# Optimization experiments

Hardware: AMD Instinct MI355X
Metric: run time of the kernel (lower is better)

The kernel has to match this reference:

```python
import jax, jax.numpy as jnp
import numpy as np

NUM_ITERATIONS = 3


def squash(s):
    # s: [..., out_channels]; norm over last axis (matches torch squash on squeezed tensor)
    norm = jnp.linalg.norm(s, axis=-1, keepdims=True)
    return (norm ** 2 / (1.0 + norm ** 2)) * (s / norm)


def setup_inputs() -> dict:
    key = jax.random.key(0)
    k1, k2 = jax.random.split(key)
    B, R, C, O, I = 256, 192, 96, 16, 20
    x = jax.random.normal(k1, (B, R, I), dtype=jnp.float32)
    W = jax.random.normal(k2, (R, C, O, I), dtype=jnp.float32)
    return {"x": x, "W": W}


def reference(x, W):
    # u_hat[b,r,c,o] = W[r,c,o,i] @ x[b,r,i]  (torch: matmul(W, x[i]) per batch element)
    u_hat = jnp.einsum('rcoi,bri->brco', W, x)  # [B,R,C,O]
    R, C = W.shape[0], W.shape[1]
    b_ij = jnp.zeros((R, C), dtype=x.dtype)  # shared across batch (torch b_ij is [1,R,C,1])
    v_j = None
    for it in range(NUM_ITERATIONS):
        c_ij = jax.nn.softmax(b_ij, axis=0)                 # softmax over routes (dim=1 in torch)
        s_j = jnp.einsum('rc,brco->bco', c_ij, u_hat)        # weighted sum over routes
        v_j = squash(s_j)                                    # [B,C,O]
        if it < NUM_ITERATIONS - 1:
            # agreement: <u_hat, v_j> averaged over batch (torch mean(dim=0))
            a_ij = jnp.einsum('brco,bco->rc', u_hat, v_j) / x.shape[0]
            b_ij = b_ij + a_ij
    return v_j  # [B, num_capsules, out_channels] (torch returns trailing singleton [B,C,O,1])
```

## Files before the change

### kernel.cpp

```cpp
#include <hip/hip_runtime.h>


#define R_ 192
#define C_ 96
#define O_ 16
#define I_ 20
#define B_ 256
#define K1 3840
#define N_ 1536
#define ZSPLIT 15
#define KCH 256
#define STILE 393216

typedef unsigned short u16;
typedef __attribute__((ext_vector_type(8))) short short8;
typedef __attribute__((ext_vector_type(4))) float floatx4;

__device__ inline float bf2f(u16 h) {
  union { unsigned int u; float f; } x; x.u = ((unsigned int)h) << 16; return x.f;
}
__device__ inline u16 f2bf(float f) {
  union { float f; unsigned int u; } x; x.f = f;
  unsigned int r = x.u + 0x7FFFu + ((x.u >> 16) & 1u);
  return (u16)(r >> 16);
}
__device__ inline unsigned int pack2(float a, float b) {
  return (unsigned int)f2bf(a) | ((unsigned int)f2bf(b) << 16);
}
__device__ inline void async16(const u16* g, u16* l) {
  __builtin_amdgcn_global_load_lds(
      (__attribute__((address_space(1))) void*)(unsigned long long)g,
      (__attribute__((address_space(3))) void*)(unsigned int)(unsigned long long)l,
      16, 0, 0);
}

__global__ void k_prep(const float* __restrict__ W, const float* __restrict__ X,
                       u16* __restrict__ WtT, u16* __restrict__ Xk,
                       u16* __restrict__ xT, float* __restrict__ bij) {
  int bid = blockIdx.x;
  if (bid < 5760) {
    int t = (bid * 256 + threadIdx.x) << 2;
    int n = t / K1, k = t - n * K1;
    int c = n >> 4, o = n & 15;
    const float* Wn = W + (size_t)(c * O_ + o) * I_;
    u16 h[4];
    #pragma unroll
    for (int e = 0; e < 4; ++e) {
      int ke = k + e, r = ke / I_, i = ke - r * I_;
      h[e] = f2bf(Wn[(size_t)r * (C_ * O_ * I_) + i]);
    }
    ushort4 o4; o4.x = h[0]; o4.y = h[1]; o4.z = h[2]; o4.w = h[3];
    *(ushort4*)&WtT[t] = o4;
  } else if (bid < 6000) {
    __shared__ u16 tile[64][72];
    int idx = bid - 5760;
    int kb = (idx % 60) << 6, bb = (idx / 60) << 6;
    int brow = threadIdx.x >> 4;
    int kq = (threadIdx.x & 15) << 2;
    #pragma unroll
    for (int p = 0; p < 4; ++p) {
      int bl = p * 16 + brow;
      float4 v = *(const float4*)(X + (size_t)(bb + bl) * K1 + kb + kq);
      ushort4 h;
      h.x = f2bf(v.x); h.y = f2bf(v.y); h.z = f2bf(v.z); h.w = f2bf(v.w);
      *(ushort4*)(Xk + (size_t)(bb + bl) * K1 + kb + kq) = h;
      tile[kq + 0][bl] = h.x;
      tile[kq + 1][bl] = h.y;
      tile[kq + 2][bl] = h.z;
      tile[kq + 3][bl] = h.w;
    }
    __syncthreads();
    int kr = threadIdx.x >> 3;
    int bq = (threadIdx.x & 7) << 3;
    #pragma unroll
    for (int q = 0; q < 2; ++q) {
      int kl = q * 32 + kr;
      *(uint4*)(xT + (size_t)(kb + kl) * B_ + bb + bq) = *(const uint4*)&tile[kl][bq];
    }
  } else {
    int t = ((bid - 6000) * 256 + threadIdx.x) << 2;
    if (t < R_ * C_) *(float4*)&bij[t] = (float4){0.f, 0.f, 0.f, 0.f};
  }
}

__device__ inline uint4 scale_b8(uint4 raw, int kg, const float* smrow) {
  int r0 = kg / I_;
  int bnd = (r0 + 1) * I_ - kg;
  float s0 = smrow[r0];
  float s1 = smrow[(r0 + 1 < R_) ? r0 + 1 : R_ - 1];
  union { uint4 q; u16 h[8]; } u; u.q = raw;
  #pragma unroll
  for (int j = 0; j < 8; ++j)
    u.h[j] = f2bf(bf2f(u.h[j]) * ((j < bnd) ? s0 : s1));
  return u.q;
}

__global__ __launch_bounds__(256) void gemm1(
    const u16* __restrict__ A, const u16* __restrict__ Bt,
    const float* __restrict__ bij, u16* __restrict__ P, int doScale) {
  __shared__ u16 As[2][2][128 * 32];
  __shared__ u16 Bs[2][2][64 * 32];
  __shared__ float sm[4][192];
  int tid = threadIdx.x;
  int w = tid >> 6, lane = tid & 63;
  if (doScale) {
    int c = (blockIdx.y << 2) + w;
    float e0 = bij[c * R_ + lane];
    float e1 = bij[c * R_ + lane + 64];
    float e2 = bij[c * R_ + lane + 128];
    float mx = fmaxf(e0, fmaxf(e1, e2));
    #pragma unroll
    for (int off = 32; off > 0; off >>= 1) mx = fmaxf(mx, __shfl_xor(mx, off));
    e0 = expf(e0 - mx); e1 = expf(e1 - mx); e2 = expf(e2 - mx);
    float s = e0 + e1 + e2;
    #pragma unroll
    for (int off = 32; off > 0; off >>= 1) s += __shfl_xor(s, off);
    float inv = 1.0f / s;
    sm[w][lane] = e0 * inv;
    sm[w][lane + 64] = e1 * inv;
    sm[w][lane + 128] = e2 * inv;
  }

  long m0 = (long)blockIdx.x * 128, n0 = (long)blockIdx.y * 64;
  int k0 = blockIdx.z * KCH;
  const u16* Ab = A + m0 * K1 + k0;
  const u16* Bb = Bt + n0 * K1 + k0;
  int srow = tid >> 2;
  int scol = (tid & 3) << 3;
  int wm = (w >> 1) << 6, wn = (w & 1) << 5;
  int quad = lane >> 4, lrow = lane & 15;
  int wb = w << 9;
  const u16* Ag0 = Ab + (long)srow * K1 + scol;
  const u16* Ag1 = Ab + (long)(srow + 64) * K1 + scol;
  const u16* Bg0 = Bb + (long)srow * K1 + scol;
  floatx4 acc[4][2];
  #pragma unroll
  for (int a = 0; a < 4; ++a)
    #pragma unroll
    for (int b = 0; b < 2; ++b) acc[a][b] = (floatx4){0.f, 0.f, 0.f, 0.f};

  async16(Ag0, &As[0][0][wb]);
  async16(Ag1, &As[0][0][2048 + wb]);
  async16(Ag0 + 32, &As[0][1][wb]);
  async16(Ag1 + 32, &As[0][1][2048 + wb]);
  uint4 b0, b1;
  if (doScale) {
    b0 = *(const uint4*)Bg0;
    b1 = *(const uint4*)(Bg0 + 32);
  } else {
    async16(Bg0, &Bs[0][0][wb]);
    async16(Bg0 + 32, &Bs[0][1][wb]);
  }
  __syncthreads();

  int p = 0;
  for (int kt = 0; kt < 4; ++kt) {
    if (doScale) {
      int kg = k0 + (kt << 6) + scol;
      ((uint4*)Bs[p][0])[tid] = scale_b8(b0, kg, &sm[w][0]);
      ((uint4*)Bs[p][1])[tid] = scale_b8(b1, kg + 32, &sm[w][0]);
      __syncthreads();
    } else if (kt > 0) {
      __syncthreads();
    }
    if (kt + 1 < 4) {
      int kk = (kt + 1) << 6;
      async16(Ag0 + kk, &As[p ^ 1][0][wb]);
      async16(Ag1 + kk, &As[p ^ 1][0][2048 + wb]);
      async16(Ag0 + kk + 32, &As[p ^ 1][1][wb]);
      async16(Ag1 + kk + 32, &As[p ^ 1][1][2048 + wb]);
      if (doScale) {
        b0 = *(const uint4*)(Bg0 + kk);
        b1 = *(const uint4*)(Bg0 + kk + 32);
      } else {
        async16(Bg0 + kk, &Bs[p ^ 1][0][wb]);
        async16(Bg0 + kk + 32, &Bs[p ^ 1][1][wb]);
      }
    }
    #pragma unroll
    for (int s = 0; s < 2; ++s) {
      short8 af[4], bfr[2];
      #pragma unroll
      for (int ms = 0; ms < 4; ++ms)
        af[ms] = *(const short8*)&As[p][s][(wm + ms * 16 + lrow) * 32 + (quad << 3)];
      #pragma unroll
      for (int ns = 0; ns < 2; ++ns)
        bfr[ns] = *(const short8*)&Bs[p][s][(wn + ns * 16 + lrow) * 32 + (quad << 3)];
      #pragma unroll
      for (int ms = 0; ms < 4; ++ms)
        #pragma unroll
        for (int ns = 0; ns < 2; ++ns)
          acc[ms][ns] = __builtin_amdgcn_mfma_f32_16x16x32_bf16(
              af[ms], bfr[ns], acc[ms][ns], 0, 0, 0);
    }
    p ^= 1;
  }
  size_t zb = (size_t)blockIdx.z * (size_t)STILE;
  #pragma unroll
  for (int ms = 0; ms < 4; ++ms)
    #pragma unroll
    for (int ns = 0; ns < 2; ++ns) {
      int b = (int)m0 + wm + ms * 16 + (quad << 2);
      int n = (int)n0 + wn + ns * 16 + lrow;
      uint2 pk;
      pk.x = pack2(acc[ms][ns][0], acc[ms][ns][1]);
      pk.y = pack2(acc[ms][ns][2], acc[ms][ns][3]);
      *(uint2*)&P[zb + (size_t)n * B_ + b] = pk;
    }
}

__global__ void k_redsq(const u16* __restrict__ P, float* __restrict__ out,
                        u16* __restrict__ vT, float preScale, int last) {
  __shared__ float nsq_l[4][64];
  int c = blockIdx.x, bh = blockIdx.y;
  int lane = threadIdx.x & 63, og = threadIdx.x >> 6;
  int b = (bh << 6) + lane;
  int n0 = (c << 4) + (og << 2);
  float acc[4];
  #pragma unroll
  for (int oo = 0; oo < 4; ++oo) acc[oo] = 0.f;
  #pragma unroll
  for (int z = 0; z < ZSPLIT; ++z) {
    size_t base = (size_t)z * STILE + (size_t)n0 * B_ + b;
    #pragma unroll
    for (int oo = 0; oo < 4; ++oo)
      acc[oo] += bf2f(P[base + (size_t)oo * B_]);
  }
  #pragma unroll
  for (int oo = 0; oo < 4; ++oo) acc[oo] *= preScale;
  float q = acc[0] * acc[0] + acc[1] * acc[1] + acc[2] * acc[2] + acc[3] * acc[3];
  nsq_l[og][lane] = q;
  __syncthreads();
  float nsq = nsq_l[0][lane] + nsq_l[1][lane] + nsq_l[2][lane] + nsq_l[3][lane];
  float f = nsq / ((1.0f + nsq) * sqrtf(nsq));
  #pragma unroll
  for (int oo = 0; oo < 4; ++oo) acc[oo] *= f;
  if (last) {
    *(float4*)(out + (size_t)b * N_ + n0) = (float4){acc[0], acc[1], acc[2], acc[3]};
  } else {
    #pragma unroll
    for (int oo = 0; oo < 4; ++oo)
      vT[(size_t)(n0 + oo) * B_ + b] = f2bf(acc[oo]);
  }
}

__global__ __launch_bounds__(256) void gemm2_agree(
    const u16* __restrict__ A, const u16* __restrict__ Bt,
    const u16* __restrict__ WtT, float* __restrict__ bij) {
  const int K = 256;
  __shared__ u16 As[2][2][128 * 32];
  __shared__ u16 Bs[2][2][64 * 32];
  int tid = threadIdx.x;
  long m0 = (long)blockIdx.x * 128, n0 = (long)blockIdx.y * 64;
  const u16* Ab = A + m0 * K;
  const u16* Bb = Bt + n0 * K;
  int srow = tid >> 2;
  int scol = (tid & 3) << 3;
  int w = tid >> 6, lane = tid & 63;
  int wm = (w >> 1) << 6, wn = (w & 1) << 5;
  int quad = lane >> 4, lrow = lane & 15;
  int wb = w << 9;
  const u16* Ag0 = Ab + (long)srow * K + scol;
  const u16* Ag1 = Ab + (long)(srow + 64) * K + scol;
  const u16* Bg0 = Bb + (long)srow * K + scol;
  floatx4 acc[4][2];
  #pragma unroll
  for (int a = 0; a < 4; ++a)
    #pragma unroll
    for (int b = 0; b < 2; ++b) acc[a][b] = (floatx4){0.f, 0.f, 0.f, 0.f};

  async16(Ag0, &As[0][0][wb]);
  async16(Ag1, &As[0][0][2048 + wb]);
  async16(Ag0 + 32, &As[0][1][wb]);
  async16(Ag1 + 32, &As[0][1][2048 + wb]);
  async16(Bg0, &Bs[0][0][wb]);
  async16(Bg0 + 32, &Bs[0][1][wb]);

  int p = 0;
  #pragma unroll
  for (int kt = 0; kt < 4; ++kt) {
    __syncthreads();
    if (kt + 1 < 4) {
      int kk = (kt + 1) << 6;
      async16(Ag0 + kk, &As[p ^ 1][0][wb]);
      async16(Ag1 + kk, &As[p ^ 1][0][2048 + wb]);
      async16(Ag0 + kk + 32, &As[p ^ 1][1][wb]);
      async16(Ag1 + kk + 32, &As[p ^ 1][1][2048 + wb]);
      async16(Bg0 + kk, &Bs[p ^ 1][0][wb]);
      async16(Bg0 + kk + 32, &Bs[p ^ 1][1][wb]);
    }
    #pragma unroll
    for (int s = 0; s < 2; ++s) {
      short8 af[4], bfr[2];
      #pragma unroll
      for (int ms = 0; ms < 4; ++ms)
        af[ms] = *(const short8*)&As[p][s][(wm + ms * 16 + lrow) * 32 + (quad << 3)];
      #pragma unroll
      for (int ns = 0; ns < 2; ++ns)
        bfr[ns] = *(const short8*)&Bs[p][s][(wn + ns * 16 + lrow) * 32 + (quad << 3)];
      #pragma unroll
      for (int ms = 0; ms < 4; ++ms)
        #pragma unroll
        for (int ns = 0; ns < 2; ++ns)
          acc[ms][ns] = __builtin_amdgcn_mfma_f32_16x16x32_bf16(
              af[ms], bfr[ns], acc[ms][ns], 0, 0, 0);
    }
    p ^= 1;
  }
  #pragma unroll
  for (int ms = 0; ms < 4; ++ms) {
    int rowbase = (int)m0 + wm + ms * 16;
    int r_lo = rowbase / I_;
    int r_hi = (rowbase + 15) / I_;
    int bnd = (r_lo + 1) * I_;
    int rowl = rowbase + (quad << 2);
    #pragma unroll
    for (int ns = 0; ns < 2; ++ns) {
      int col = (int)n0 + wn + ns * 16 + lrow;
      uint2 wv = *(const uint2*)&WtT[(size_t)col * K1 + rowl];
      u16 h[4];
      h[0] = (u16)(wv.x & 0xffff); h[1] = (u16)(wv.x >> 16);
      h[2] = (u16)(wv.y & 0xffff); h[3] = (u16)(wv.y >> 16);
      float p0 = 0.f, p1 = 0.f;
      #pragma unroll
      for (int e = 0; e < 4; ++e) {
        float pr = acc[ms][ns][e] * bf2f(h[e]);
        if (rowl + e < bnd) p0 += pr; else p1 += pr;
      }
      #pragma unroll
      for (int off = 32; off > 0; off >>= 1) {
        p0 += __shfl_xor(p0, off);
        p1 += __shfl_xor(p1, off);
      }
      if (lane == 0) {
        int c = col >> 4;
        atomicAdd(&bij[c * R_ + r_lo], p0 * (1.0f / 256.0f));
        atomicAdd(&bij[c * R_ + r_hi], p1 * (1.0f / 256.0f));
      }
    }
  }
}

extern "C" void kernel_launch(void* const* d_in, const int* in_sizes, int n_in,
                              void* d_out, int out_size, void* d_ws, size_t ws_size,
                              hipStream_t stream) {
  const float* X = (const float*)d_in[0];
  const float* W = (const float*)d_in[1];
  float* out = (float*)d_out;
  char* ws = (char*)d_ws;
  u16*  WtT = (u16*)(ws);
  u16*  Xk  = (u16*)(ws + 11796480);
  u16*  xT  = (u16*)(ws + 13762560);
  u16*  vT  = (u16*)(ws + 15728640);
  u16*  Pb  = (u16*)(ws + 16515072);
  float* bij = (float*)(ws + 28311552);

  k_prep<<<6018, 256, 0, stream>>>(W, X, WtT, Xk, xT, bij);

  for (int it = 0; it < 3; ++it) {
    gemm1<<<dim3(2, 24, ZSPLIT), 256, 0, stream>>>(Xk, WtT, bij, Pb, it > 0);
    k_redsq<<<dim3(96, 4), 256, 0, stream>>>(
        Pb, out, vT, it == 0 ? (1.0f / 192.0f) : 1.0f, it == 2);
    if (it < 2)
      gemm2_agree<<<dim3(30, 24), 256, 0, stream>>>(xT, vT, WtT, bij);
  }
}
```

Before: 149.7 us.

## Fuse split-K reduction and squash into gemm1 via last-block atomic counter

Removes the separate k_redsq kernel. Each gemm1 block bumps a per-tile atomic counter after writing its partial tile, and the last of the ZSPLIT blocks for that tile sums all partials, applies squash through shared memory, and writes either the output or vT. This cuts three kernel launches and their gaps, but the final reduction now runs on only 48 blocks. It adds a shared-memory union, a threadfence and atomics, and sets launch bounds to ask for 3 blocks per CU.

```diff
diff --git a/kernel.cpp b/kernel.cpp
--- a/kernel.cpp
+++ b/kernel.cpp
@@ -36,7 +36,8 @@
 
 __global__ void k_prep(const float* __restrict__ W, const float* __restrict__ X,
                        u16* __restrict__ WtT, u16* __restrict__ Xk,
-                       u16* __restrict__ xT, float* __restrict__ bij) {
+                       u16* __restrict__ xT, float* __restrict__ bij,
+                       int* __restrict__ cnt) {
   int bid = blockIdx.x;
   if (bid < 5760) {
     int t = (bid * 256 + threadIdx.x) << 2;
@@ -77,9 +78,11 @@
       int kl = q * 32 + kr;
       *(uint4*)(xT + (size_t)(kb + kl) * B_ + bb + bq) = *(const uint4*)&tile[kl][bq];
     }
-  } else {
+  } else if (bid < 6018) {
     int t = ((bid - 6000) * 256 + threadIdx.x) << 2;
     if (t < R_ * C_) *(float4*)&bij[t] = (float4){0.f, 0.f, 0.f, 0.f};
+  } else {
+    if (threadIdx.x < 3 * 48) cnt[threadIdx.x] = 0;
   }
 }
 
@@ -95,12 +98,23 @@
   return u.q;
 }
 
-__global__ __launch_bounds__(256) void gemm1(
+__global__ __launch_bounds__(256, 3) void gemm1(
     const u16* __restrict__ A, const u16* __restrict__ Bt,
-    const float* __restrict__ bij, u16* __restrict__ P, int doScale) {
-  __shared__ u16 As[2][2][128 * 32];
-  __shared__ u16 Bs[2][2][64 * 32];
-  __shared__ float sm[4][192];
+    const float* __restrict__ bij, u16* __restrict__ P, int doScale,
+    float* __restrict__ out, u16* __restrict__ vT, int* __restrict__ cnt,
+    float preScale, int last, int itIdx) {
+  __shared__ union SH {
+    struct {
+      u16 As[2][2][128 * 32];
+      u16 Bs[2][2][64 * 32];
+      float sm[4][192];
+    } g;
+    struct {
+      float s[64][129];
+      float f[4][128];
+    } r;
+  } sh;
+  __shared__ int lastFlag;
   int tid = threadIdx.x;
   int w = tid >> 6, lane = tid & 63;
   if (doScale) {
@@ -116,9 +130,9 @@
     #pragma unroll
     for (int off = 32; off > 0; off >>= 1) s += __shfl_xor(s, off);
     float inv = 1.0f / s;
-    sm[w][lane] = e0 * inv;
-    sm[w][lane + 64] = e1 * inv;
-    sm[w][lane + 128] = e2 * inv;
+    sh.g.sm[w][lane] = e0 * inv;
+    sh.g.sm[w][lane + 64] = e1 * inv;
+    sh.g.sm[w][lane + 128] = e2 * inv;
   }
 
   long m0 = (long)blockIdx.x * 128, n0 = (long)blockIdx.y * 64;
@@ -139,17 +153,17 @@
     #pragma unroll
     for (int b = 0; b < 2; ++b) acc[a][b] = (floatx4){0.f, 0.f, 0.f, 0.f};
 
-  async16(Ag0, &As[0][0][wb]);
-  async16(Ag1, &As[0][0][2048 + wb]);
-  async16(Ag0 + 32, &As[0][1][wb]);
-  async16(Ag1 + 32, &As[0][1][2048 + wb]);
+  async16(Ag0, &sh.g.As[0][0][wb]);
+  async16(Ag1, &sh.g.As[0][0][2048 + wb]);
+  async16(Ag0 + 32, &sh.g.As[0][1][wb]);
+  async16(Ag1 + 32, &sh.g.As[0][1][2048 + wb]);
   uint4 b0, b1;
   if (doScale) {
     b0 = *(const uint4*)Bg0;
     b1 = *(const uint4*)(Bg0 + 32);
   } else {
-    async16(Bg0, &Bs[0][0][wb]);
-    async16(Bg0 + 32, &Bs[0][1][wb]);
+    async16(Bg0, &sh.g.Bs[0][0][wb]);
+    async16(Bg0 + 32, &sh.g.Bs[0][1][wb]);
   }
   __syncthreads();
 
@@ -157,24 +171,24 @@
   for (int kt = 0; kt < 4; ++kt) {
     if (doScale) {
       int kg = k0 + (kt << 6) + scol;
-      ((uint4*)Bs[p][0])[tid] = scale_b8(b0, kg, &sm[w][0]);
-      ((uint4*)Bs[p][1])[tid] = scale_b8(b1, kg + 32, &sm[w][0]);
+      ((uint4*)sh.g.Bs[p][0])[tid] = scale_b8(b0, kg, &sh.g.sm[w][0]);
+      ((uint4*)sh.g.Bs[p][1])[tid] = scale_b8(b1, kg + 32, &sh.g.sm[w][0]);
       __syncthreads();
     } else if (kt > 0) {
       __syncthreads();
     }
     if (kt + 1 < 4) {
       int kk = (kt + 1) << 6;
-      async16(Ag0 + kk, &As[p ^ 1][0][wb]);
-      async16(Ag1 + kk, &As[p ^ 1][0][2048 + wb]);
-      async16(Ag0 + kk + 32, &As[p ^ 1][1][wb]);
-      async16(Ag1 + kk + 32, &As[p ^ 1][1][2048 + wb]);
+      async16(Ag0 + kk, &sh.g.As[p ^ 1][0][wb]);
+      async16(Ag1 + kk, &sh.g.As[p ^ 1][0][2048 + wb]);
+      async16(Ag0 + kk + 32, &sh.g.As[p ^ 1][1][wb]);
+      async16(Ag1 + kk + 32, &sh.g.As[p ^ 1][1][2048 + wb]);
       if (doScale) {
         b0 = *(const uint4*)(Bg0 + kk);
         b1 = *(const uint4*)(Bg0 + kk + 32);
       } else {
-        async16(Bg0 + kk, &Bs[p ^ 1][0][wb]);
-        async16(Bg0 + kk + 32, &Bs[p ^ 1][1][wb]);
+        async16(Bg0 + kk, &sh.g.Bs[p ^ 1][0][wb]);
+        async16(Bg0 + kk + 32, &sh.g.Bs[p ^ 1][1][wb]);
       }
     }
     #pragma unroll
@@ -182,10 +196,10 @@
       short8 af[4], bfr[2];
       #pragma unroll
       for (int ms = 0; ms < 4; ++ms)
-        af[ms] = *(const short8*)&As[p][s][(wm + ms * 16 + lrow) * 32 + (quad << 3)];
+        af[ms] = *(const short8*)&sh.g.As[p][s][(wm + ms * 16 + lrow) * 32 + (quad << 3)];
       #pragma unroll
       for (int ns = 0; ns < 2; ++ns)
-        bfr[ns] = *(const short8*)&Bs[p][s][(wn + ns * 16 + lrow) * 32 + (quad << 3)];
+        bfr[ns] = *(const short8*)&sh.g.Bs[p][s][(wn + ns * 16 + lrow) * 32 + (quad << 3)];
       #pragma unroll
       for (int ms = 0; ms < 4; ++ms)
         #pragma unroll
@@ -207,40 +221,81 @@
       pk.y = pack2(acc[ms][ns][2], acc[ms][ns][3]);
       *(uint2*)&P[zb + (size_t)n * B_ + b] = pk;
     }
-}
-
-__global__ void k_redsq(const u16* __restrict__ P, float* __restrict__ out,
-                        u16* __restrict__ vT, float preScale, int last) {
-  __shared__ float nsq_l[4][64];
-  int c = blockIdx.x, bh = blockIdx.y;
-  int lane = threadIdx.x & 63, og = threadIdx.x >> 6;
-  int b = (bh << 6) + lane;
-  int n0 = (c << 4) + (og << 2);
-  float acc[4];
-  #pragma unroll
-  for (int oo = 0; oo < 4; ++oo) acc[oo] = 0.f;
-  #pragma unroll
-  for (int z = 0; z < ZSPLIT; ++z) {
-    size_t base = (size_t)z * STILE + (size_t)n0 * B_ + b;
-    #pragma unroll
-    for (int oo = 0; oo < 4; ++oo)
-      acc[oo] += bf2f(P[base + (size_t)oo * B_]);
-  }
-  #pragma unroll
-  for (int oo = 0; oo < 4; ++oo) acc[oo] *= preScale;
-  float q = acc[0] * acc[0] + acc[1] * acc[1] + acc[2] * acc[2] + acc[3] * acc[3];
-  nsq_l[og][lane] = q;
+
+  __threadfence();
   __syncthreads();
-  float nsq = nsq_l[0][lane] + nsq_l[1][lane] + nsq_l[2][lane] + nsq_l[3][lane];
-  float f = nsq / ((1.0f + nsq) * sqrtf(nsq));
-  #pragma unroll
-  for (int oo = 0; oo < 4; ++oo) acc[oo] *= f;
+  if (tid == 0) {
+    int old = atomicAdd(&cnt[itIdx * 48 + (int)blockIdx.x * 24 + (int)blockIdx.y], 1);
+    lastFlag = (old == ZSPLIT - 1) ? 1 : 0;
+  }
+  __syncthreads();
+  if (!lastFlag) return;
+  __threadfence();
+
+  int tb = (int)m0, tn = (int)n0;
+  #pragma unroll
+  for (int k = 0; k < 4; ++k) {
+    int task = tid + (k << 8);
+    int n = task >> 4, bg = task & 15;
+    const u16* base = P + (size_t)(tn + n) * B_ + tb + (bg << 3);
+    float a[8];
+    #pragma unroll
+    for (int j = 0; j < 8; ++j) a[j] = 0.f;
+    for (int z = 0; z < ZSPLIT; ++z) {
+      union { uint4 q; u16 h[8]; } u;
+      u.q = *(const uint4*)(base + (size_t)z * STILE);
+      #pragma unroll
+      for (int j = 0; j < 8; ++j) a[j] += bf2f(u.h[j]);
+    }
+    #pragma unroll
+    for (int j = 0; j < 8; ++j) sh.r.s[n][(bg << 3) + j] = a[j] * preScale;
+  }
+  __syncthreads();
+  {
+    int cB = tid >> 6, bb = tid & 63;
+    #pragma unroll
+    for (int hh = 0; hh < 2; ++hh) {
+      int b = bb + (hh << 6);
+      float nsq = 0.f;
+      #pragma unroll
+      for (int o = 0; o < 16; ++o) {
+        float v = sh.r.s[(cB << 4) + o][b];
+        nsq += v * v;
+      }
+      sh.r.f[cB][b] = nsq / ((1.0f + nsq) * sqrtf(nsq));
+    }
+  }
+  __syncthreads();
   if (last) {
-    *(float4*)(out + (size_t)b * N_ + n0) = (float4){acc[0], acc[1], acc[2], acc[3]};
+    #pragma unroll
+    for (int k = 0; k < 8; ++k) {
+      int task = tid + (k << 8);
+      int bl = task >> 4, nq = task & 15;
+      int n = nq << 2, cc = n >> 4;
+      float fv = sh.r.f[cc][bl];
+      float4 v;
+      v.x = sh.r.s[n + 0][bl] * fv;
+      v.y = sh.r.s[n + 1][bl] * fv;
+      v.z = sh.r.s[n + 2][bl] * fv;
+      v.w = sh.r.s[n + 3][bl] * fv;
+      *(float4*)(out + (size_t)(tb + bl) * N_ + tn + n) = v;
+    }
   } else {
     #pragma unroll
-    for (int oo = 0; oo < 4; ++oo)
-      vT[(size_t)(n0 + oo) * B_ + b] = f2bf(acc[oo]);
+    for (int k = 0; k < 4; ++k) {
+      int task = tid + (k << 8);
+      int n = task >> 4, bg = task & 15;
+      int cc = n >> 4, bs = bg << 3;
+      uint4 o4;
+      unsigned int* po = (unsigned int*)&o4;
+      #pragma unroll
+      for (int j = 0; j < 4; ++j) {
+        float lo = sh.r.s[n][bs + 2 * j] * sh.r.f[cc][bs + 2 * j];
+        float hi = sh.r.s[n][bs + 2 * j + 1] * sh.r.f[cc][bs + 2 * j + 1];
+        po[j] = pack2(lo, hi);
+      }
+      *(uint4*)&vT[(size_t)(tn + n) * B_ + tb + bs] = o4;
+    }
   }
 }
 
@@ -354,13 +409,14 @@
   u16*  vT  = (u16*)(ws + 15728640);
   u16*  Pb  = (u16*)(ws + 16515072);
   float* bij = (float*)(ws + 28311552);
-
-  k_prep<<<6018, 256, 0, stream>>>(W, X, WtT, Xk, xT, bij);
+  int*  cnt = (int*)(ws + 28385280);
+
+  k_prep<<<6019, 256, 0, stream>>>(W, X, WtT, Xk, xT, bij, cnt);
 
   for (int it = 0; it < 3; ++it) {
-    gemm1<<<dim3(2, 24, ZSPLIT), 256, 0, stream>>>(Xk, WtT, bij, Pb, it > 0);
-    k_redsq<<<dim3(96, 4), 256, 0, stream>>>(
-        Pb, out, vT, it == 0 ? (1.0f / 192.0f) : 1.0f, it == 2);
+    gemm1<<<dim3(2, 24, ZSPLIT), 256, 0, stream>>>(
+        Xk, WtT, bij, Pb, it > 0, out, vT, cnt,
+        it == 0 ? (1.0f / 192.0f) : 1.0f, it == 2 ? 1 : 0, it);
     if (it < 2)
       gemm2_agree<<<dim3(30, 24), 256, 0, stream>>>(xT, vT, WtT, bij);
   }
```

New measurement: 459.3 us. +206.9%, slower.

## Fuse split-K reduction and squash into gemm1 using small full-K tiles

Applied to the files above, without the earlier changes.

Replaces the split-K gemm1 (15 K chunks written as bf16 partials) plus the separate reduce-and-squash kernel with a single gemm1 that computes full K per 32x32 tile. The squash norm is done in-register with lane shuffles across the 16 output channels. This removes one launch per iteration and the partial-sum buffer traffic, and avoids rounding partials to bf16. In exchange each block now runs a long 30-step serial K loop doing one MFMA per LDS stage, with only 384 blocks, so per-block latency and low MFMA density may dominate.

```diff
diff --git a/kernel.cpp b/kernel.cpp
--- a/kernel.cpp
+++ b/kernel.cpp
@@ -8,9 +8,7 @@
 #define B_ 256
 #define K1 3840
 #define N_ 1536
-#define ZSPLIT 15
-#define KCH 256
-#define STILE 393216
+#define NKT 30
 
 typedef unsigned short u16;
 typedef __attribute__((ext_vector_type(8))) short short8;
@@ -97,14 +95,16 @@
 
 __global__ __launch_bounds__(256) void gemm1(
     const u16* __restrict__ A, const u16* __restrict__ Bt,
-    const float* __restrict__ bij, u16* __restrict__ P, int doScale) {
-  __shared__ u16 As[2][2][128 * 32];
-  __shared__ u16 Bs[2][2][64 * 32];
-  __shared__ float sm[4][192];
+    const float* __restrict__ bij, int doScale,
+    float* __restrict__ out, u16* __restrict__ vT,
+    float preScale, int last) {
+  __shared__ u16 As[2][4][1024];
+  __shared__ u16 Bs[2][4][1024];
+  __shared__ float sm[2][192];
   int tid = threadIdx.x;
   int w = tid >> 6, lane = tid & 63;
-  if (doScale) {
-    int c = (blockIdx.y << 2) + w;
+  if (doScale && w < 2) {
+    int c = ((int)blockIdx.x << 1) + w;
     float e0 = bij[c * R_ + lane];
     float e1 = bij[c * R_ + lane + 64];
     float e2 = bij[c * R_ + lane + 128];
@@ -121,126 +121,93 @@
     sm[w][lane + 128] = e2 * inv;
   }
 
-  long m0 = (long)blockIdx.x * 128, n0 = (long)blockIdx.y * 64;
-  int k0 = blockIdx.z * KCH;
-  const u16* Ab = A + m0 * K1 + k0;
-  const u16* Bb = Bt + n0 * K1 + k0;
-  int srow = tid >> 2;
-  int scol = (tid & 3) << 3;
-  int wm = (w >> 1) << 6, wn = (w & 1) << 5;
+  long n0 = (long)blockIdx.x * 32, m0 = (long)blockIdx.y * 32;
+  const u16* Ab = A + m0 * K1;
+  const u16* Bb = Bt + n0 * K1;
+  int srow = ((w & 1) << 4) + (lane >> 2);
+  int scol = (lane & 3) << 3;
+  int subA = w >> 1;
+  int rb = (w & 1) << 9;
+  const u16* Ag = Ab + (long)srow * K1 + subA * 32 + scol;
+  const u16* Bg = Bb + (long)srow * K1 + subA * 32 + scol;
+  int rowb = tid >> 3;
+  int kc = (tid & 7) << 3;
+  const u16* Bgs = Bb + (long)rowb * K1 + kc;
+  const float* smrow = &sm[rowb >> 4][0];
+  int wm = (w >> 1) << 4, wn = (w & 1) << 4;
   int quad = lane >> 4, lrow = lane & 15;
-  int wb = w << 9;
-  const u16* Ag0 = Ab + (long)srow * K1 + scol;
-  const u16* Ag1 = Ab + (long)(srow + 64) * K1 + scol;
-  const u16* Bg0 = Bb + (long)srow * K1 + scol;
-  floatx4 acc[4][2];
-  #pragma unroll
-  for (int a = 0; a < 4; ++a)
-    #pragma unroll
-    for (int b = 0; b < 2; ++b) acc[a][b] = (floatx4){0.f, 0.f, 0.f, 0.f};
-
-  async16(Ag0, &As[0][0][wb]);
-  async16(Ag1, &As[0][0][2048 + wb]);
-  async16(Ag0 + 32, &As[0][1][wb]);
-  async16(Ag1 + 32, &As[0][1][2048 + wb]);
-  uint4 b0, b1;
+  floatx4 acc = (floatx4){0.f, 0.f, 0.f, 0.f};
+
+  async16(Ag, &As[0][subA][rb]);
+  async16(Ag + 64, &As[0][subA + 2][rb]);
+  uint4 pb0, pb1;
   if (doScale) {
-    b0 = *(const uint4*)Bg0;
-    b1 = *(const uint4*)(Bg0 + 32);
+    pb0 = *(const uint4*)Bgs;
+    pb1 = *(const uint4*)(Bgs + 64);
   } else {
-    async16(Bg0, &Bs[0][0][wb]);
-    async16(Bg0 + 32, &Bs[0][1][wb]);
+    async16(Bg, &Bs[0][subA][rb]);
+    async16(Bg + 64, &Bs[0][subA + 2][rb]);
   }
   __syncthreads();
 
   int p = 0;
-  for (int kt = 0; kt < 4; ++kt) {
+  for (int kt = 0; kt < NKT; ++kt) {
     if (doScale) {
-      int kg = k0 + (kt << 6) + scol;
-      ((uint4*)Bs[p][0])[tid] = scale_b8(b0, kg, &sm[w][0]);
-      ((uint4*)Bs[p][1])[tid] = scale_b8(b1, kg + 32, &sm[w][0]);
+      int kg = (kt << 7) + kc;
+      int sub = kc >> 5;
+      *(uint4*)&Bs[p][sub][rowb * 32 + (kc & 31)] = scale_b8(pb0, kg, smrow);
+      *(uint4*)&Bs[p][sub + 2][rowb * 32 + (kc & 31)] = scale_b8(pb1, kg + 64, smrow);
       __syncthreads();
     } else if (kt > 0) {
       __syncthreads();
     }
-    if (kt + 1 < 4) {
-      int kk = (kt + 1) << 6;
-      async16(Ag0 + kk, &As[p ^ 1][0][wb]);
-      async16(Ag1 + kk, &As[p ^ 1][0][2048 + wb]);
-      async16(Ag0 + kk + 32, &As[p ^ 1][1][wb]);
-      async16(Ag1 + kk + 32, &As[p ^ 1][1][2048 + wb]);
+    if (kt + 1 < NKT) {
+      int kk = (kt + 1) << 7;
+      async16(Ag + kk, &As[p ^ 1][subA][rb]);
+      async16(Ag + kk + 64, &As[p ^ 1][subA + 2][rb]);
       if (doScale) {
-        b0 = *(const uint4*)(Bg0 + kk);
-        b1 = *(const uint4*)(Bg0 + kk + 32);
+        pb0 = *(const uint4*)(Bgs + kk);
+        pb1 = *(const uint4*)(Bgs + kk + 64);
       } else {
-        async16(Bg0 + kk, &Bs[p ^ 1][0][wb]);
-        async16(Bg0 + kk + 32, &Bs[p ^ 1][1][wb]);
+        async16(Bg + kk, &Bs[p ^ 1][subA][rb]);
+        async16(Bg + kk + 64, &Bs[p ^ 1][subA + 2][rb]);
       }
     }
     #pragma unroll
-    for (int s = 0; s < 2; ++s) {
-      short8 af[4], bfr[2];
-      #pragma unroll
-      for (int ms = 0; ms < 4; ++ms)
-        af[ms] = *(const short8*)&As[p][s][(wm + ms * 16 + lrow) * 32 + (quad << 3)];
-      #pragma unroll
-      for (int ns = 0; ns < 2; ++ns)
-        bfr[ns] = *(const short8*)&Bs[p][s][(wn + ns * 16 + lrow) * 32 + (quad << 3)];
-      #pragma unroll
-      for (int ms = 0; ms < 4; ++ms)
-        #pragma unroll
-        for (int ns = 0; ns < 2; ++ns)
-          acc[ms][ns] = __builtin_amdgcn_mfma_f32_16x16x32_bf16(
-              af[ms], bfr[ns], acc[ms][ns], 0, 0, 0);
+    for (int s = 0; s < 4; ++s) {
+      short8 af = *(const short8*)&As[p][s][(wm + lrow) * 32 + (quad << 3)];
+      short8 bfr = *(const short8*)&Bs[p][s][(wn + lrow) * 32 + (quad << 3)];
+      acc = __builtin_amdgcn_mfma_f32_16x16x32_bf16(af, bfr, acc, 0, 0, 0);
     }
     p ^= 1;
   }
-  size_t zb = (size_t)blockIdx.z * (size_t)STILE;
-  #pragma unroll
-  for (int ms = 0; ms < 4; ++ms)
-    #pragma unroll
-    for (int ns = 0; ns < 2; ++ns) {
-      int b = (int)m0 + wm + ms * 16 + (quad << 2);
-      int n = (int)n0 + wn + ns * 16 + lrow;
-      uint2 pk;
-      pk.x = pack2(acc[ms][ns][0], acc[ms][ns][1]);
-      pk.y = pack2(acc[ms][ns][2], acc[ms][ns][3]);
-      *(uint2*)&P[zb + (size_t)n * B_ + b] = pk;
-    }
-}
-
-__global__ void k_redsq(const u16* __restrict__ P, float* __restrict__ out,
-                        u16* __restrict__ vT, float preScale, int last) {
-  __shared__ float nsq_l[4][64];
-  int c = blockIdx.x, bh = blockIdx.y;
-  int lane = threadIdx.x & 63, og = threadIdx.x >> 6;
-  int b = (bh << 6) + lane;
-  int n0 = (c << 4) + (og << 2);
-  float acc[4];
-  #pragma unroll
-  for (int oo = 0; oo < 4; ++oo) acc[oo] = 0.f;
-  #pragma unroll
-  for (int z = 0; z < ZSPLIT; ++z) {
-    size_t base = (size_t)z * STILE + (size_t)n0 * B_ + b;
-    #pragma unroll
-    for (int oo = 0; oo < 4; ++oo)
-      acc[oo] += bf2f(P[base + (size_t)oo * B_]);
-  }
-  #pragma unroll
-  for (int oo = 0; oo < 4; ++oo) acc[oo] *= preScale;
-  float q = acc[0] * acc[0] + acc[1] * acc[1] + acc[2] * acc[2] + acc[3] * acc[3];
-  nsq_l[og][lane] = q;
-  __syncthreads();
-  float nsq = nsq_l[0][lane] + nsq_l[1][lane] + nsq_l[2][lane] + nsq_l[3][lane];
-  float f = nsq / ((1.0f + nsq) * sqrtf(nsq));
-  #pragma unroll
-  for (int oo = 0; oo < 4; ++oo) acc[oo] *= f;
+
+  float v0 = acc[0] * preScale, v1 = acc[1] * preScale;
+  float v2 = acc[2] * preScale, v3 = acc[3] * preScale;
+  float q0 = v0 * v0, q1 = v1 * v1, q2 = v2 * v2, q3 = v3 * v3;
+  #pragma unroll
+  for (int off = 1; off < 16; off <<= 1) {
+    q0 += __shfl_xor(q0, off);
+    q1 += __shfl_xor(q1, off);
+    q2 += __shfl_xor(q2, off);
+    q3 += __shfl_xor(q3, off);
+  }
+  v0 *= q0 / ((1.0f + q0) * sqrtf(q0));
+  v1 *= q1 / ((1.0f + q1) * sqrtf(q1));
+  v2 *= q2 / ((1.0f + q2) * sqrtf(q2));
+  v3 *= q3 / ((1.0f + q3) * sqrtf(q3));
+  int n = (int)n0 + wn + lrow;
+  int b = (int)m0 + wm + (quad << 2);
   if (last) {
-    *(float4*)(out + (size_t)b * N_ + n0) = (float4){acc[0], acc[1], acc[2], acc[3]};
+    out[(size_t)(b + 0) * N_ + n] = v0;
+    out[(size_t)(b + 1) * N_ + n] = v1;
+    out[(size_t)(b + 2) * N_ + n] = v2;
+    out[(size_t)(b + 3) * N_ + n] = v3;
   } else {
-    #pragma unroll
-    for (int oo = 0; oo < 4; ++oo)
-      vT[(size_t)(n0 + oo) * B_ + b] = f2bf(acc[oo]);
+    uint2 pk;
+    pk.x = pack2(v0, v1);
+    pk.y = pack2(v2, v3);
+    *(uint2*)&vT[(size_t)n * B_ + b] = pk;
   }
 }
 
@@ -352,15 +319,14 @@
   u16*  Xk  = (u16*)(ws + 11796480);
   u16*  xT  = (u16*)(ws + 13762560);
   u16*  vT  = (u16*)(ws + 15728640);
-  u16*  Pb  = (u16*)(ws + 16515072);
-  float* bij = (float*)(ws + 28311552);
+  float* bij = (float*)(ws + 16515072);
 
   k_prep<<<6018, 256, 0, stream>>>(W, X, WtT, Xk, xT, bij);
 
   for (int it = 0; it < 3; ++it) {
-    gemm1<<<dim3(2, 24, ZSPLIT), 256, 0, stream>>>(Xk, WtT, bij, Pb, it > 0);
-    k_redsq<<<dim3(96, 4), 256, 0, stream>>>(
-        Pb, out, vT, it == 0 ? (1.0f / 192.0f) : 1.0f, it == 2);
+    gemm1<<<dim3(48, 8), 256, 0, stream>>>(
+        Xk, WtT, bij, it > 0, out, vT,
+        it == 0 ? (1.0f / 192.0f) : 1.0f, it == 2 ? 1 : 0);
     if (it < 2)
       gemm2_agree<<<dim3(30, 24), 256, 0, stream>>>(xT, vT, WtT, bij);
   }
```

Measured after the change: 173.6 us. 16.0% more time.
